# Kernel tuning notes

Measured on AMD Instinct MI355X. Metric: run time of the kernel, lower is better.

Reference implementation:

```python
import jax, jax.numpy as jnp
import numpy as np

B, L, D = 2, 2048, 2048
N, K, H = 16, 8, 128
EPS = 1e-6
ROPE_THETA = 1000000
K_MASK = -2.3819763e+38


def rms_norm(x, w, eps=EPS):
    dtype = x.dtype
    rms = jnp.sqrt(jnp.mean(x.astype(jnp.float32) ** 2, axis=-1, keepdims=True) + eps)
    return (w * x / rms).astype(dtype)


def apply_rope(inputs, positions, head_dim, rope_theta=ROPE_THETA):
    # inputs: [B, L, n, H], positions: [B, L]
    fraction = 2 * jnp.arange(0, head_dim // 2, dtype=jnp.float32) / head_dim
    timescale = rope_theta ** fraction  # [H/2]
    sinusoid = positions[..., jnp.newaxis] / timescale[jnp.newaxis, jnp.newaxis, :]  # [B,L,H/2]
    sinusoid = sinusoid[..., jnp.newaxis, :]  # [B,L,1,H/2]
    sin, cos = jnp.sin(sinusoid), jnp.cos(sinusoid)
    first, second = jnp.split(inputs, 2, axis=-1)
    out = jnp.concatenate([first * cos - second * sin, second * cos + first * sin], axis=-1)
    return out.astype(inputs.dtype)


def setup_inputs() -> dict:
    key = jax.random.key(0)
    ks = jax.random.split(key, 6)
    x = jax.random.normal(ks[0], (B, L, D), dtype=jnp.float32)
    position_ids = jnp.broadcast_to(jnp.arange(L, dtype=jnp.int32)[None, :], (B, L))
    # causal mask [B, L, S]
    attn_mask = jnp.broadcast_to(jnp.tril(jnp.ones((L, L), dtype=bool))[None], (B, L, L))
    wq = jax.random.normal(ks[1], (D, N, H), dtype=jnp.float32) * 0.02
    wk = jax.random.normal(ks[2], (D, K, H), dtype=jnp.float32) * 0.02
    wv = jax.random.normal(ks[3], (D, K, H), dtype=jnp.float32) * 0.02
    wo = jax.random.normal(ks[4], (N, H, D), dtype=jnp.float32) * 0.02
    q_norm_w = jnp.ones((H,), dtype=jnp.float32)
    k_norm_w = jnp.ones((H,), dtype=jnp.float32)
    return {"x": x, "position_ids": position_ids, "attn_mask": attn_mask,
            "wq": wq, "wk": wk, "wv": wv, "wo": wo,
            "q_norm_w": q_norm_w, "k_norm_w": k_norm_w}


def reference(x, position_ids, attn_mask, wq, wk, wv, wo, q_norm_w, k_norm_w):
    scale = H ** (-0.5)
    q = jnp.einsum('BLD,DNH->BLNH', x, wq)  # [B,L,N,H]
    k = jnp.einsum('BSD,DKH->BSKH', x, wk)  # [B,S,K,H]
    v = jnp.einsum('BSD,DKH->BSKH', x, wv)
    q = rms_norm(q, q_norm_w)
    k = rms_norm(k, k_norm_w)
    q = apply_rope(q, position_ids, H)
    k = apply_rope(k, position_ids, H)
    b, l, n, h = q.shape
    s = k.shape[1]
    kk = k.shape[2]
    q = q.reshape((b, l, kk, n // kk, h))
    attn = jnp.einsum('BLKGH,BSKH->BKGLS', q, k) * scale
    attn = attn.reshape((b, n, l, s))
    attn = jnp.where(jnp.expand_dims(attn_mask, -3), attn, K_MASK)
    attn = jax.nn.softmax(attn.astype(jnp.float32), axis=-1).astype(k.dtype)
    attn = attn.reshape((b, kk, n // kk, l, s))
    qkv = jnp.einsum('BKGLS,BSKH->BLKGH', attn, v).reshape((b, l, n, h))
    out = jnp.einsum('BLNH,NHD->BLD', qkv, wo)
    return out
```

## Files before the change

### kernel.cpp

```cpp
#include <hip/hip_runtime.h>

#define B_ 2
#define L_ 2048
#define D_ 2048
#define NH_ 16
#define KH_ 8
#define HD_ 128

typedef __attribute__((ext_vector_type(8))) short short8;
typedef __attribute__((ext_vector_type(4))) short short4v;
typedef __attribute__((ext_vector_type(4))) float floatx4;

__device__ __forceinline__ unsigned short f2bf(float f) {
  unsigned u = __float_as_uint(f);
  unsigned r = (u + 0x7fffu + ((u >> 16) & 1u)) >> 16;
  return (unsigned short)r;
}
__device__ __forceinline__ float bf2f(unsigned short h) {
  return __uint_as_float(((unsigned)h) << 16);
}
__device__ __forceinline__ void gl_lds16(const void* g, void* l) {
  __builtin_amdgcn_global_load_lds(
      (const __attribute__((address_space(1))) unsigned int*)g,
      (__attribute__((address_space(3))) unsigned int*)l, 16, 0, 0);
}
__device__ __forceinline__ void barrier_lds_only() {
  asm volatile("s_waitcnt lgkmcnt(0)" ::: "memory");
  __builtin_amdgcn_s_barrier();
}

__global__ __launch_bounds__(256) void prep1(const float* __restrict__ x,
                                             const float* __restrict__ wq,
                                             const float* __restrict__ wk,
                                             const float* __restrict__ wv,
                                             const float* __restrict__ wo,
                                             unsigned short* __restrict__ xb,
                                             unsigned short* __restrict__ wqkv_t,
                                             unsigned short* __restrict__ wo_t) {
  int id = blockIdx.x;
  int t = threadIdx.x;
  if (id < 8192) {
    long i = ((long)id * 256 + t) * 4;
    float4 v = *(const float4*)(x + i);
    ushort4 o;
    o.x = f2bf(v.x); o.y = f2bf(v.y); o.z = f2bf(v.z); o.w = f2bf(v.w);
    *(ushort4*)(xb + i) = o;
    return;
  }
  id -= 8192;
  __shared__ float tile[32][33];
  const float* in;
  unsigned short* out;
  int C, sh;
  if (id < 4096) {
    in = wq; out = wqkv_t; C = 2048; sh = 6;
  } else if (id < 6144) {
    in = wk; out = wqkv_t + 2048L * 2048; C = 1024; sh = 5; id -= 4096;
  } else if (id < 8192) {
    in = wv; out = wqkv_t + 3072L * 2048; C = 1024; sh = 5; id -= 6144;
  } else {
    in = wo; out = wo_t; C = 2048; sh = 6; id -= 8192;
  }
  int c0 = (id & ((1 << sh) - 1)) * 32, r0 = (id >> sh) * 32;
  int tx = t & 31, ty = t >> 5;
#pragma unroll
  for (int i = 0; i < 4; i++)
    tile[ty + i * 8][tx] = in[(long)(r0 + ty + i * 8) * C + c0 + tx];
  __syncthreads();
#pragma unroll
  for (int i = 0; i < 4; i++) {
    int oc = ty + i * 8;
    out[(long)(c0 + oc) * 2048 + r0 + tx] = f2bf(tile[tx][oc]);
  }
}

template <int MODE>
__global__ __launch_bounds__(256, 3) void gemm128(const unsigned short* __restrict__ A,
                                                  const unsigned short* __restrict__ Bt,
                                                  void* __restrict__ C,
                                                  int M, int N, int K) {
  __shared__ unsigned short As[128 * 64];
  __shared__ unsigned short Bs[128 * 64];
  const int t = threadIdx.x;
  const int lane = t & 63, w = t >> 6;
  const int wy = w >> 1, wx = w & 1;
  const int col = lane & 15, quad = lane >> 4;
  const long m0 = (long)blockIdx.y * 128, n0 = (long)blockIdx.x * 128;
  floatx4 acc[4][4];
#pragma unroll
  for (int i = 0; i < 4; i++)
#pragma unroll
    for (int j = 0; j < 4; j++) acc[i][j] = (floatx4)0.0f;
  const int rs = t >> 3, bs = t & 7;
  for (int kt = 0; kt < K; kt += 64) {
#pragma unroll
    for (int i = 0; i < 4; i++) {
      int r = i * 32 + rs;
      gl_lds16(A + (m0 + r) * (long)K + kt + ((bs ^ (r & 7)) << 3),
               &As[(i * 32 + w * 8) * 64]);
      gl_lds16(Bt + (n0 + r) * (long)K + kt + ((bs ^ (r & 7)) << 3),
               &Bs[(i * 32 + w * 8) * 64]);
    }
    __syncthreads();
#pragma unroll
    for (int ks = 0; ks < 2; ks++) {
      short8 af[4], bf[4];
#pragma unroll
      for (int mi = 0; mi < 4; mi++) {
        int row = wy * 64 + mi * 16 + col;
        int blk = ks * 4 + quad;
        af[mi] = *(const short8*)&As[row * 64 + ((blk ^ (row & 7)) << 3)];
      }
#pragma unroll
      for (int ni = 0; ni < 4; ni++) {
        int row = wx * 64 + ni * 16 + col;
        int blk = ks * 4 + quad;
        bf[ni] = *(const short8*)&Bs[row * 64 + ((blk ^ (row & 7)) << 3)];
      }
#pragma unroll
      for (int mi = 0; mi < 4; mi++)
#pragma unroll
        for (int ni = 0; ni < 4; ni++)
          acc[mi][ni] = __builtin_amdgcn_mfma_f32_16x16x32_bf16(af[mi], bf[ni],
                                                                acc[mi][ni], 0, 0, 0);
    }
    __syncthreads();
  }
#pragma unroll
  for (int mi = 0; mi < 4; mi++)
#pragma unroll
    for (int r = 0; r < 4; r++) {
      long row = m0 + wy * 64 + mi * 16 + quad * 4 + r;
#pragma unroll
      for (int ni = 0; ni < 4; ni++) {
        long cg = n0 + wx * 64 + ni * 16 + col;
        float val = acc[mi][ni][r];
        if (MODE == 1)
          ((unsigned short*)C)[row * N + cg] = f2bf(val);
        else
          ((float*)C)[row * N + cg] = val;
      }
    }
}

template <int MODE>
__global__ __launch_bounds__(512, 2) void gemm256(const unsigned short* __restrict__ A,
                                                  const unsigned short* __restrict__ Bt,
                                                  void* __restrict__ C,
                                                  int M, int N, int K,
                                                  unsigned short* __restrict__ qptr,
                                                  unsigned short* __restrict__ kptr,
                                                  unsigned short* __restrict__ vTptr,
                                                  const int* __restrict__ posp,
                                                  const float* __restrict__ qwp,
                                                  const float* __restrict__ kwp) {
  __shared__ unsigned short SMu[4][256 * 64];
  const int t = threadIdx.x;
  const int lane = t & 63, w = t >> 6;
  const int wy = w >> 2, wx = w & 3;
  const int col = lane & 15, quad = lane >> 4;
  const long m0 = (long)blockIdx.y * 256, n0 = (long)blockIdx.x * 256;
  const int rs = t >> 3, bs = t & 7;
  const int nt = K >> 6;

#define SA256(bufi, Tt, h)                                                      \
  gl_lds16(A + (m0 + (h) * 64 + rs) * (long)K + (long)(Tt) * 64 +               \
               ((bs ^ (rs & 7)) << 3),                                          \
           &SMu[bufi][((h) * 64 + w * 8) * 64])
#define SB256(bufi, Tt, h)                                                      \
  gl_lds16(Bt + (n0 + (h) * 64 + rs) * (long)K + (long)(Tt) * 64 +              \
                ((bs ^ (rs & 7)) << 3),                                         \
           &SMu[2 + (bufi)][((h) * 64 + w * 8) * 64])

  floatx4 acc[8][4];
#pragma unroll
  for (int i = 0; i < 8; i++)
#pragma unroll
    for (int j = 0; j < 4; j++) acc[i][j] = (floatx4)0.0f;

  SA256(0, 0, 0); SA256(0, 0, 1); SA256(0, 0, 2); SA256(0, 0, 3);
  SB256(0, 0, 0); SB256(0, 0, 1); SB256(0, 0, 2); SB256(0, 0, 3);
  SB256(1, 1, 0); SB256(1, 1, 1); SB256(1, 1, 2); SB256(1, 1, 3);
  asm volatile("s_waitcnt vmcnt(4)" ::: "memory");
  __builtin_amdgcn_s_barrier();

  for (int T = 0; T < nt; ++T) {
    const int c = T & 1;
    const unsigned short* Ac = SMu[c];
    const unsigned short* Bc = SMu[2 + c];
    short8 a[4][2], b[4][2];

#pragma unroll
    for (int mi = 0; mi < 4; mi++)
#pragma unroll
      for (int ks = 0; ks < 2; ks++) {
        int row = wy * 128 + mi * 16 + col;
        a[mi][ks] = *(const short8*)&Ac[row * 64 + (((ks * 4 + quad) ^ (row & 7)) << 3)];
      }
#pragma unroll
    for (int ni = 0; ni < 2; ni++)
#pragma unroll
      for (int ks = 0; ks < 2; ks++) {
        int row = wx * 64 + ni * 16 + col;
        b[ni][ks] = *(const short8*)&Bc[row * 64 + (((ks * 4 + quad) ^ (row & 7)) << 3)];
      }
    if (T + 1 < nt) { SA256(c ^ 1, T + 1, 0); SA256(c ^ 1, T + 1, 2); }
    __builtin_amdgcn_s_barrier();
    asm volatile("s_waitcnt lgkmcnt(0)" ::: "memory");
    __builtin_amdgcn_s_setprio(1);
#pragma unroll
    for (int mi = 0; mi < 4; mi++)
#pragma unroll
      for (int ni = 0; ni < 2; ni++)
#pragma unroll
        for (int ks = 0; ks < 2; ks++)
          acc[mi][ni] = __builtin_amdgcn_mfma_f32_16x16x32_bf16(a[mi][ks], b[ni][ks],
                                                                acc[mi][ni], 0, 0, 0);
    __builtin_amdgcn_s_setprio(0);
    __builtin_amdgcn_s_barrier();

#pragma unroll
    for (int ni = 2; ni < 4; ni++)
#pragma unroll
      for (int ks = 0; ks < 2; ks++) {
        int row = wx * 64 + ni * 16 + col;
        b[ni][ks] = *(const short8*)&Bc[row * 64 + (((ks * 4 + quad) ^ (row & 7)) << 3)];
      }
    if (T + 1 < nt) { SA256(c ^ 1, T + 1, 1); SA256(c ^ 1, T + 1, 3); }
    __builtin_amdgcn_s_barrier();
    asm volatile("s_waitcnt lgkmcnt(0)" ::: "memory");
    __builtin_amdgcn_s_setprio(1);
#pragma unroll
    for (int mi = 0; mi < 4; mi++)
#pragma unroll
      for (int ni = 2; ni < 4; ni++)
#pragma unroll
        for (int ks = 0; ks < 2; ks++)
          acc[mi][ni] = __builtin_amdgcn_mfma_f32_16x16x32_bf16(a[mi][ks], b[ni][ks],
                                                                acc[mi][ni], 0, 0, 0);
    __builtin_amdgcn_s_setprio(0);
    __builtin_amdgcn_s_barrier();

#pragma unroll
    for (int mi = 0; mi < 4; mi++)
#pragma unroll
      for (int ks = 0; ks < 2; ks++) {
        int row = wy * 128 + (mi + 4) * 16 + col;
        a[mi][ks] = *(const short8*)&Ac[row * 64 + (((ks * 4 + quad) ^ (row & 7)) << 3)];
      }
    if (T + 2 < nt) { SB256(c, T + 2, 0); SB256(c, T + 2, 1); }
    __builtin_amdgcn_s_barrier();
    asm volatile("s_waitcnt lgkmcnt(0)" ::: "memory");
    __builtin_amdgcn_s_setprio(1);
#pragma unroll
    for (int mi = 0; mi < 4; mi++)
#pragma unroll
      for (int ni = 0; ni < 2; ni++)
#pragma unroll
        for (int ks = 0; ks < 2; ks++)
          acc[mi + 4][ni] = __builtin_amdgcn_mfma_f32_16x16x32_bf16(a[mi][ks], b[ni][ks],
                                                                    acc[mi + 4][ni], 0, 0, 0);
    __builtin_amdgcn_s_setprio(0);
    __builtin_amdgcn_s_barrier();

    if (T + 2 < nt) { SB256(c, T + 2, 2); SB256(c, T + 2, 3); }
    __builtin_amdgcn_s_setprio(1);
#pragma unroll
    for (int mi = 0; mi < 4; mi++)
#pragma unroll
      for (int ni = 2; ni < 4; ni++)
#pragma unroll
        for (int ks = 0; ks < 2; ks++)
          acc[mi + 4][ni] = __builtin_amdgcn_mfma_f32_16x16x32_bf16(a[mi][ks], b[ni][ks],
                                                                    acc[mi + 4][ni], 0, 0, 0);
    __builtin_amdgcn_s_setprio(0);
    if (T + 1 < nt) {
      if (T >= nt - 2)
        asm volatile("s_waitcnt vmcnt(0)" ::: "memory");
      else
        asm volatile("s_waitcnt vmcnt(4)" ::: "memory");
      __builtin_amdgcn_s_barrier();
    }
  }
#undef SA256
#undef SB256

  if (MODE == 2) {
    const int bx = blockIdx.x;
    const int bb = (int)(m0 >> 11);
    const int l0r = (int)(m0 & 2047);
    __syncthreads();

    if (bx >= 12) {
      const int khb = (bx - 12) * 2;
      unsigned short* Vt = (unsigned short*)SMu;
#pragma unroll
      for (int mi = 0; mi < 8; mi++)
#pragma unroll
        for (int ni = 0; ni < 4; ni++) {
          int cc = wx * 64 + ni * 16 + col;
          int rbase = wy * 128 + mi * 16 + quad * 4;
          short4v pk;
#pragma unroll
          for (int r = 0; r < 4; r++) pk[r] = (short)f2bf(acc[mi][ni][r]);
          *(short4v*)&Vt[cc * 256 + (rbase ^ ((cc & 15) << 4))] = pk;
        }
      __syncthreads();
      for (int i = 0; i < 32; i++) {
        int cc = w * 32 + i;
        int hloc = cc & 127;
        int khh = khb + (cc >> 7);
        ushort4 v4 = *(const ushort4*)&Vt[cc * 256 + ((lane * 4) ^ ((cc & 15) << 4))];
        *(ushort4*)&vTptr[(((long)bb * KH_ + khh) * HD_ + hloc) * (long)L_ + l0r + lane * 4] = v4;
      }
      return;
    }

    const bool isq = (bx < 8);
    const float* nwp = isq ? qwp : kwp;
    float* PART = (float*)SMu;
#pragma unroll
    for (int mi = 0; mi < 8; mi++)
#pragma unroll
      for (int r = 0; r < 4; r++) {
        float s = acc[mi][0][r] * acc[mi][0][r] + acc[mi][1][r] * acc[mi][1][r] +
                  acc[mi][2][r] * acc[mi][2][r] + acc[mi][3][r] * acc[mi][3][r];
        s += __shfl_xor(s, 1);
        s += __shfl_xor(s, 2);
        s += __shfl_xor(s, 4);
        s += __shfl_xor(s, 8);
        if (col == 0)
          PART[((wy * 128 + mi * 16 + quad * 4 + r) << 2) + wx] = s;
      }
    __syncthreads();
    float inv[8][4];
    {
      const int wp = (wx >> 1) << 1;
#pragma unroll
      for (int mi = 0; mi < 8; mi++)
#pragma unroll
        for (int r = 0; r < 4; r++) {
          int lr = wy * 128 + mi * 16 + quad * 4 + r;
          float ss = PART[(lr << 2) + wp] + PART[(lr << 2) + wp + 1];
          inv[mi][r] = 1.0f / sqrtf(ss * (1.0f / 128.0f) + 1e-6f);
        }
    }
    __syncthreads();
    float* plane = (float*)SMu;
    const float nw0 = nwp[lane], nw1 = nwp[lane + 64];
    const float QSC = 0.08838834764831845f * 1.4426950408889634f;
    for (int hh = 0; hh < 2; hh++) {
      if (wy == hh) {
#pragma unroll
        for (int mi = 0; mi < 8; mi++)
#pragma unroll
          for (int ni = 0; ni < 4; ni++) {
            int cc = wx * 64 + ni * 16 + col;
#pragma unroll
            for (int r = 0; r < 4; r++)
              plane[(mi * 16 + quad * 4 + r) * 256 + cc] = acc[mi][ni][r] * inv[mi][r];
          }
      }
      __syncthreads();
      for (int i = 0; i < 16; i++) {
        int lr = w * 16 + i;
        int lg = l0r + hh * 128 + lr;
        float x0a = plane[lr * 256 + lane];
        float x1a = plane[lr * 256 + lane + 64];
        float x0b = plane[lr * 256 + 128 + lane];
        float x1b = plane[lr * 256 + 192 + lane];
        float p = (float)posp[bb * L_ + lg];
        float ang = p * exp2f((float)lane * -0.31143075889f);
        float sv, cv;
        sincosf(ang, &sv, &cv);
        x0a *= nw0; x1a *= nw1; x0b *= nw0; x1b *= nw1;
        float o0a = x0a * cv - x1a * sv, o1a = x1a * cv + x0a * sv;
        float o0b = x0b * cv - x1b * sv, o1b = x1b * cv + x0b * sv;
        unsigned short* d0;
        if (isq) {
          o0a *= QSC; o1a *= QSC; o0b *= QSC; o1b *= QSC;
          d0 = qptr + (((long)bb * NH_ + bx * 2) * L_ + lg) * HD_;
        } else {
          d0 = kptr + (((long)bb * KH_ + (bx - 8) * 2) * L_ + lg) * HD_;
        }
        d0[lane] = f2bf(o0a);
        d0[lane + 64] = f2bf(o1a);
        d0[(long)L_ * HD_ + lane] = f2bf(o0b);
        d0[(long)L_ * HD_ + lane + 64] = f2bf(o1b);
      }
      __syncthreads();
    }
    return;
  }

#pragma unroll
  for (int mi = 0; mi < 8; mi++)
#pragma unroll
    for (int r = 0; r < 4; r++) {
      long row = m0 + wy * 128 + mi * 16 + quad * 4 + r;
#pragma unroll
      for (int ni = 0; ni < 4; ni++) {
        long cg = n0 + wx * 64 + ni * 16 + col;
        float val = acc[mi][ni][r];
        if (MODE == 1)
          ((unsigned short*)C)[row * N + cg] = f2bf(val);
        else
          ((float*)C)[row * N + cg] = val;
      }
    }
}

__global__ __launch_bounds__(256, 2) void flash(const unsigned short* __restrict__ Q,
                                                const unsigned short* __restrict__ Kg,
                                                const unsigned short* __restrict__ VT,
                                                unsigned short* __restrict__ Og) {
  __shared__ unsigned short Ks[64 * 128];
  __shared__ unsigned short Vs[128 * 64];
  __shared__ unsigned short Ps[128 * 72];
  const int n = blockIdx.y, b = blockIdx.z;
  const int qt = b ? (15 - blockIdx.x) : blockIdx.x;
  const int t = threadIdx.x, lane = t & 63, w = t >> 6;
  const int col = lane & 15, quad = lane >> 4;
  const int kvh = n >> 1;
  const unsigned short* kb = Kg + ((long)b * KH_ + kvh) * L_ * HD_;
  const unsigned short* vtb = VT + ((long)b * KH_ + kvh) * HD_ * L_;
  const int l0 = qt * 128;
  const int steps = 2 * qt + 2;
  const unsigned short* qb = Q + (((long)b * NH_ + n) * L_ + l0) * HD_;

  const int rK = t >> 4, blkK = t & 15;
  const int rV = t >> 3, blkV = t & 7;

  short8 qf[2][4];
#pragma unroll
  for (int mi = 0; mi < 2; mi++)
#pragma unroll
    for (int ks = 0; ks < 4; ks++)
      qf[mi][ks] = *(const short8*)(qb + (w * 32 + mi * 16 + col) * 128 + ks * 32 + quad * 8);

  floatx4 o[2][8];
#pragma unroll
  for (int mi = 0; mi < 2; mi++)
#pragma unroll
    for (int nf = 0; nf < 8; nf++) o[mi][nf] = (floatx4)0.0f;
  float lrowA[2] = {0.0f, 0.0f}, lrowB[2] = {0.0f, 0.0f};

  {
#pragma unroll
    for (int i = 0; i < 4; i++) {
      int r = i * 16 + rK;
      int gblk = (blkK & 8) | ((blkK ^ r) & 7);
      gl_lds16(kb + (long)r * 128 + gblk * 8, &Ks[(i * 16 + w * 4) * 128]);
    }
#pragma unroll
    for (int j = 0; j < 4; j++) {
      int r = j * 32 + rV;
      int gblk = (blkV ^ r) & 7;
      gl_lds16(vtb + (long)r * L_ + gblk * 8, &Vs[(j * 32 + w * 8) * 64]);
    }
  }
  __syncthreads();

  short8 kpre[4], vpre[4];
  if (steps > 1) {
    const int s0n = 64;
#pragma unroll
    for (int i = 0; i < 4; i++) {
      int r = i * 16 + rK;
      int gblk = (blkK & 8) | ((blkK ^ r) & 7);
      kpre[i] = *(const short8*)(kb + (long)(s0n + r) * 128 + gblk * 8);
    }
#pragma unroll
    for (int j = 0; j < 4; j++) {
      int r = j * 32 + rV;
      int gblk = (blkV ^ r) & 7;
      vpre[j] = *(const short8*)(vtb + (long)r * L_ + s0n + gblk * 8);
    }
  }

  for (int st = 0; st < steps; st++) {
    const int s0 = st * 64;
    floatx4 sa[2][4];
#pragma unroll
    for (int mi = 0; mi < 2; mi++)
#pragma unroll
      for (int sf = 0; sf < 4; sf++) sa[mi][sf] = (floatx4)0.0f;
#pragma unroll
    for (int ks = 0; ks < 4; ks++) {
      short8 bf[4];
#pragma unroll
      for (int sf = 0; sf < 4; sf++) {
        int srow = sf * 16 + col;
        int blk = ks * 4 + quad;
        bf[sf] = *(const short8*)&Ks[srow * 128 + (((blk & 8) | ((blk ^ srow) & 7)) << 3)];
      }
#pragma unroll
      for (int mi = 0; mi < 2; mi++)
#pragma unroll
        for (int sf = 0; sf < 4; sf++)
          sa[mi][sf] = __builtin_amdgcn_mfma_f32_16x16x32_bf16(bf[sf], qf[mi][ks],
                                                               sa[mi][sf], 0, 0, 0);
    }

    if (st >= steps - 2) {
#pragma unroll
      for (int mi = 0; mi < 2; mi++) {
        int lg = l0 + w * 32 + mi * 16 + col;
#pragma unroll
        for (int sf = 0; sf < 4; sf++)
#pragma unroll
          for (int r = 0; r < 4; r++) {
            int sg = s0 + sf * 16 + quad * 4 + r;
            if (sg > lg) sa[mi][sf][r] = -3.0e38f;
          }
      }
    }

#pragma unroll
    for (int mi = 0; mi < 2; mi++)
#pragma unroll
      for (int sf = 0; sf < 4; sf++) {
        float p0 = exp2f(sa[mi][sf][0] - 17.0f);
        float p1 = exp2f(sa[mi][sf][1] - 17.0f);
        float p2 = exp2f(sa[mi][sf][2] - 17.0f);
        float p3 = exp2f(sa[mi][sf][3] - 17.0f);
        lrowA[mi] += p0 + p1;
        lrowB[mi] += p2 + p3;
        short4v pk;
        pk[0] = (short)f2bf(p0);
        pk[1] = (short)f2bf(p1);
        pk[2] = (short)f2bf(p2);
        pk[3] = (short)f2bf(p3);
        *(short4v*)&Ps[(w * 32 + mi * 16 + col) * 72 + sf * 16 + quad * 4] = pk;
      }

#pragma unroll
    for (int ks = 0; ks < 2; ks++) {
      short8 pf[2];
#pragma unroll
      for (int mi = 0; mi < 2; mi++)
        pf[mi] = *(const short8*)&Ps[(w * 32 + mi * 16 + col) * 72 + ks * 32 + quad * 8];
      short8 vf[8];
#pragma unroll
      for (int nf = 0; nf < 8; nf++) {
        int h = nf * 16 + col;
        int blk = ks * 4 + quad;
        vf[nf] = *(const short8*)&Vs[h * 64 + ((blk ^ (h & 7)) << 3)];
      }
#pragma unroll
      for (int mi = 0; mi < 2; mi++)
#pragma unroll
        for (int nf = 0; nf < 8; nf++)
          o[mi][nf] = __builtin_amdgcn_mfma_f32_16x16x32_bf16(pf[mi], vf[nf],
                                                              o[mi][nf], 0, 0, 0);
    }

    barrier_lds_only();
    if (st + 1 < steps) {
#pragma unroll
      for (int i = 0; i < 4; i++) {
        int r = i * 16 + rK;
        *(short8*)&Ks[r * 128 + blkK * 8] = kpre[i];
      }
#pragma unroll
      for (int j = 0; j < 4; j++) {
        int r = j * 32 + rV;
        *(short8*)&Vs[r * 64 + blkV * 8] = vpre[j];
      }
      barrier_lds_only();
      if (st + 2 < steps) {
        const int s0n = (st + 2) * 64;
#pragma unroll
        for (int i = 0; i < 4; i++) {
          int r = i * 16 + rK;
          int gblk = (blkK & 8) | ((blkK ^ r) & 7);
          kpre[i] = *(const short8*)(kb + (long)(s0n + r) * 128 + gblk * 8);
        }
#pragma unroll
        for (int j = 0; j < 4; j++) {
          int r = j * 32 + rV;
          int gblk = (blkV ^ r) & 7;
          vpre[j] = *(const short8*)(vtb + (long)r * L_ + s0n + gblk * 8);
        }
      }
    }
  }

#pragma unroll
  for (int mi = 0; mi < 2; mi++) {
    float s = lrowA[mi] + lrowB[mi];
    s += __shfl_xor(s, 16);
    s += __shfl_xor(s, 32);
#pragma unroll
    for (int r = 0; r < 4; r++) {
      float inv = 1.0f / __shfl(s, quad * 4 + r);
      int lg = l0 + w * 32 + mi * 16 + quad * 4 + r;
      unsigned short* dst = Og + (((long)b * L_ + lg) * NH_ + n) * HD_;
#pragma unroll
      for (int nf = 0; nf < 8; nf++)
        dst[nf * 16 + col] = f2bf(o[mi][nf][r] * inv);
    }
  }
}

extern "C" void kernel_launch(void* const* d_in, const int* in_sizes, int n_in,
                              void* d_out, int out_size, void* d_ws, size_t ws_size,
                              hipStream_t stream) {
  const float* x = (const float*)d_in[0];
  const int* pos = (const int*)d_in[1];
  const float* wq = (const float*)d_in[3];
  const float* wk = (const float*)d_in[4];
  const float* wv = (const float*)d_in[5];
  const float* wo = (const float*)d_in[6];
  const float* qnw = (const float*)d_in[7];
  const float* knw = (const float*)d_in[8];
  float* out = (float*)d_out;

  char* ws = (char*)d_ws;
  unsigned short* xb     = (unsigned short*)(ws + 0);
  unsigned short* wqkv_t = (unsigned short*)(ws + 16777216);
  unsigned short* wo_t   = (unsigned short*)(ws + 33554432);
  unsigned short* q      = (unsigned short*)(ws + 75497472);
  unsigned short* k      = (unsigned short*)(ws + 92274688);
  unsigned short* vT     = (unsigned short*)(ws + 100663296);
  unsigned short* ao     = (unsigned short*)(ws + 109051904);
  if (ws_size < 125829120) return;

  prep1<<<20480, 256, 0, stream>>>(x, wq, wk, wv, wo, xb, wqkv_t, wo_t);
  gemm256<2><<<dim3(16, 16), 512, 0, stream>>>(xb, wqkv_t, nullptr, 4096, 4096, 2048,
                                               q, k, vT, pos, qnw, knw);
  flash<<<dim3(16, NH_, B_), 256, 0, stream>>>(q, k, vT, ao);
  gemm128<0><<<dim3(16, 32), 256, 0, stream>>>(ao, wo_t, out, 4096, 2048, 2048);
}
```

Baseline: 336.1 us.

## Double-buffer K/V shared tiles and XOR-swizzle the P buffer in flash attention

```diff
diff --git a/kernel.cpp b/kernel.cpp
--- a/kernel.cpp
+++ b/kernel.cpp
@@ -414,9 +414,9 @@
                                                 const unsigned short* __restrict__ Kg,
                                                 const unsigned short* __restrict__ VT,
                                                 unsigned short* __restrict__ Og) {
-  __shared__ unsigned short Ks[64 * 128];
-  __shared__ unsigned short Vs[128 * 64];
-  __shared__ unsigned short Ps[128 * 72];
+  __shared__ unsigned short Ks[2][64 * 128];
+  __shared__ unsigned short Vs[2][128 * 64];
+  __shared__ unsigned short Ps[128 * 64];
   const int n = blockIdx.y, b = blockIdx.z;
   const int qt = b ? (15 - blockIdx.x) : blockIdx.x;
   const int t = threadIdx.x, lane = t & 63, w = t >> 6;
@@ -430,6 +430,7 @@
 
   const int rK = t >> 4, blkK = t & 15;
   const int rV = t >> 3, blkV = t & 7;
+  const int pswz = (col & 7) << 3;
 
   short8 qf[2][4];
 #pragma unroll
@@ -450,13 +451,13 @@
     for (int i = 0; i < 4; i++) {
       int r = i * 16 + rK;
       int gblk = (blkK & 8) | ((blkK ^ r) & 7);
-      gl_lds16(kb + (long)r * 128 + gblk * 8, &Ks[(i * 16 + w * 4) * 128]);
+      gl_lds16(kb + (long)r * 128 + gblk * 8, &Ks[0][(i * 16 + w * 4) * 128]);
     }
 #pragma unroll
     for (int j = 0; j < 4; j++) {
       int r = j * 32 + rV;
       int gblk = (blkV ^ r) & 7;
-      gl_lds16(vtb + (long)r * L_ + gblk * 8, &Vs[(j * 32 + w * 8) * 64]);
+      gl_lds16(vtb + (long)r * L_ + gblk * 8, &Vs[0][(j * 32 + w * 8) * 64]);
     }
   }
   __syncthreads();
@@ -480,6 +481,10 @@
 
   for (int st = 0; st < steps; st++) {
     const int s0 = st * 64;
+    const int cur = st & 1;
+    const unsigned short* Kc = Ks[cur];
+    const unsigned short* Vc = Vs[cur];
+
     floatx4 sa[2][4];
 #pragma unroll
     for (int mi = 0; mi < 2; mi++)
@@ -492,7 +497,7 @@
       for (int sf = 0; sf < 4; sf++) {
         int srow = sf * 16 + col;
         int blk = ks * 4 + quad;
-        bf[sf] = *(const short8*)&Ks[srow * 128 + (((blk & 8) | ((blk ^ srow) & 7)) << 3)];
+        bf[sf] = *(const short8*)&Kc[srow * 128 + (((blk & 8) | ((blk ^ srow) & 7)) << 3)];
       }
 #pragma unroll
       for (int mi = 0; mi < 2; mi++)
@@ -531,21 +536,24 @@
         pk[1] = (short)f2bf(p1);
         pk[2] = (short)f2bf(p2);
         pk[3] = (short)f2bf(p3);
-        *(short4v*)&Ps[(w * 32 + mi * 16 + col) * 72 + sf * 16 + quad * 4] = pk;
+        int row = w * 32 + mi * 16 + col;
+        *(short4v*)&Ps[(row * 64 + sf * 16 + quad * 4) ^ pswz] = pk;
       }
 
 #pragma unroll
     for (int ks = 0; ks < 2; ks++) {
       short8 pf[2];
 #pragma unroll
-      for (int mi = 0; mi < 2; mi++)
-        pf[mi] = *(const short8*)&Ps[(w * 32 + mi * 16 + col) * 72 + ks * 32 + quad * 8];
+      for (int mi = 0; mi < 2; mi++) {
+        int row = w * 32 + mi * 16 + col;
+        pf[mi] = *(const short8*)&Ps[(row * 64 + ks * 32 + quad * 8) ^ pswz];
+      }
       short8 vf[8];
 #pragma unroll
       for (int nf = 0; nf < 8; nf++) {
         int h = nf * 16 + col;
         int blk = ks * 4 + quad;
-        vf[nf] = *(const short8*)&Vs[h * 64 + ((blk ^ (h & 7)) << 3)];
+        vf[nf] = *(const short8*)&Vc[h * 64 + ((blk ^ (h & 7)) << 3)];
       }
 #pragma unroll
       for (int mi = 0; mi < 2; mi++)
@@ -555,19 +563,18 @@
                                                               o[mi][nf], 0, 0, 0);
     }
 
-    barrier_lds_only();
     if (st + 1 < steps) {
+      const int nb = cur ^ 1;
 #pragma unroll
       for (int i = 0; i < 4; i++) {
         int r = i * 16 + rK;
-        *(short8*)&Ks[r * 128 + blkK * 8] = kpre[i];
+        *(short8*)&Ks[nb][r * 128 + blkK * 8] = kpre[i];
       }
 #pragma unroll
       for (int j = 0; j < 4; j++) {
         int r = j * 32 + rV;
-        *(short8*)&Vs[r * 64 + blkV * 8] = vpre[j];
-      }
-      barrier_lds_only();
+        *(short8*)&Vs[nb][r * 64 + blkV * 8] = vpre[j];
+      }
       if (st + 2 < steps) {
         const int s0n = (st + 2) * 64;
 #pragma unroll
@@ -583,6 +590,7 @@
           vpre[j] = *(const short8*)(vtb + (long)r * L_ + s0n + gblk * 8);
         }
       }
+      barrier_lds_only();
     }
   }
 
```

Measured after the change: 331.9 us. Within noise of the previous version (-1.2%).
